# Optimization experiments

Hardware: AMD Instinct MI355X
Metric: run time of the kernel (lower is better)

## Reference

```python
import jax, jax.numpy as jnp
import numpy as np

EPS = 1e-5

def _bn(x, gamma, beta):
    # BatchNorm1d forward (batch statistics, biased variance) over node dim
    mu = x.mean(axis=0)
    var = x.var(axis=0)
    return gamma * (x - mu) * jax.lax.rsqrt(var + EPS) + beta

def _gcn_conv(x, W, b, src, dst, n):
    # PyG GCNConv: h = x @ W; symmetric norm with self-loops; scatter-add to dst
    h = x @ W                                   # [N, out]
    ones = jnp.ones(src.shape, dtype=h.dtype)
    deg = jax.ops.segment_sum(ones, dst, num_segments=n) + 1.0  # +1 self-loop
    dinv = jax.lax.rsqrt(deg)                   # deg >= 1 always
    norm = dinv[src] * dinv[dst]                # [E]
    agg = jax.ops.segment_sum(h[src] * norm[:, None], dst, num_segments=n)
    agg = agg + h * (dinv * dinv)[:, None]      # self-loop contribution
    return agg + b

def setup_inputs() -> dict:
    key = jax.random.key(0)
    ks = jax.random.split(key, 10)
    N, E = 100000, 1600000
    Din, Dh, Dout = 256, 128, 128
    e_prev = jax.random.normal(ks[0], (N, Din), dtype=jnp.float32)
    edge_index = jax.random.randint(ks[1], (2, E), 0, N, dtype=jnp.int64)
    proj_W = jax.random.normal(ks[2], (Din, Din), dtype=jnp.float32) * 0.02
    proj_b = jnp.zeros((Din,), dtype=jnp.float32)
    W1 = jax.random.normal(ks[3], (Din, Dh), dtype=jnp.float32) * 0.05
    b1 = jnp.zeros((Dh,), dtype=jnp.float32)
    gamma1 = jnp.ones((Dh,), dtype=jnp.float32)
    beta1 = jnp.zeros((Dh,), dtype=jnp.float32)
    W2 = jax.random.normal(ks[4], (Dh, Dout), dtype=jnp.float32) * 0.05
    b2 = jnp.zeros((Dout,), dtype=jnp.float32)
    gamma2 = jnp.ones((Dout,), dtype=jnp.float32)
    beta2 = jnp.zeros((Dout,), dtype=jnp.float32)
    return {"e_prev": e_prev, "edge_index": edge_index,
            "proj_W": proj_W, "proj_b": proj_b,
            "W1": W1, "b1": b1, "gamma1": gamma1, "beta1": beta1,
            "W2": W2, "b2": b2, "gamma2": gamma2, "beta2": beta2}

def reference(e_prev, edge_index, proj_W, proj_b, W1, b1, gamma1, beta1, W2, b2, gamma2, beta2):
    n = e_prev.shape[0]
    src, dst = edge_index[0], edge_index[1]
    # input_projection (input_dim != hidden_dim branch)
    x = e_prev @ proj_W + proj_b
    x = _gcn_conv(x, W1, b1, src, dst, n)
    x = _bn(x, gamma1, beta1)
    x = jax.nn.relu(x)
    # dropout(0.2) is identity in eval mode
    x = _gcn_conv(x, W2, b2, src, dst, n)
    x = _bn(x, gamma2, beta2)
    return x
```

## Files before the change

kernel.cpp:

```cpp
#include <hip/hip_runtime.h>
#include <hip/hip_bf16.h>
#include <math.h>

#define BN_EPS 1e-5f
#define CAP 6144
#define MAXB 512

typedef __attribute__((ext_vector_type(8))) short short8;
typedef __attribute__((ext_vector_type(4))) float floatx4;

__device__ inline float4 ntload4(const float* p) {
    floatx4 v = __builtin_nontemporal_load((const floatx4*)p);
    return make_float4(v.x, v.y, v.z, v.w);
}

__global__ __launch_bounds__(128) void prep_kernel(
    const float* __restrict__ PW, const float* __restrict__ W1,
    const float* __restrict__ pb, const float* __restrict__ W2,
    __hip_bfloat16* __restrict__ Wf1, __hip_bfloat16* __restrict__ Wf2,
    float* __restrict__ bc, int* __restrict__ bcursor, int nb)
{
    int bid = blockIdx.x;
    int tid = threadIdx.x;
    if (bid < 256) {
        int k = bid, c = tid;
        float a0 = 0.f, a1 = 0.f, a2 = 0.f, a3 = 0.f;
        for (int kk = 0; kk < 256; kk += 4) {
            a0 = fmaf(PW[k * 256 + kk],     W1[(kk)     * 128 + c], a0);
            a1 = fmaf(PW[k * 256 + kk + 1], W1[(kk + 1) * 128 + c], a1);
            a2 = fmaf(PW[k * 256 + kk + 2], W1[(kk + 2) * 128 + c], a2);
            a3 = fmaf(PW[k * 256 + kk + 3], W1[(kk + 3) * 128 + c], a3);
        }
        float acc = (a0 + a1) + (a2 + a3);
        int kc = k >> 5, r5 = k & 31, qq = r5 >> 3, j = r5 & 7;
        int ct = c >> 4, l16 = c & 15;
        int lane = qq * 16 + l16;
        Wf1[(((kc * 8 + ct) * 64) + lane) * 8 + j] = __float2bfloat16(acc);
    } else if (bid == 256) {
        int c = tid;
        float a0 = 0.f, a1 = 0.f, a2 = 0.f, a3 = 0.f;
        for (int k = 0; k < 256; k += 4) {
            a0 = fmaf(pb[k],     W1[(k)     * 128 + c], a0);
            a1 = fmaf(pb[k + 1], W1[(k + 1) * 128 + c], a1);
            a2 = fmaf(pb[k + 2], W1[(k + 2) * 128 + c], a2);
            a3 = fmaf(pb[k + 3], W1[(k + 3) * 128 + c], a3);
        }
        bc[c] = (a0 + a1) + (a2 + a3);
    } else if (bid < 385) {
        int t = (bid - 257) * 128 + tid;
        int j    = t & 7;
        int lane = (t >> 3) & 63;
        int ct   = (t >> 9) & 7;
        int kc   = t >> 12;
        int k = kc * 32 + ((lane >> 4) & 3) * 8 + j;
        int c = ct * 16 + (lane & 15);
        Wf2[t] = __float2bfloat16(W2[k * 128 + c]);
    } else {
        int i = (bid - 385) * 128 + tid;
        if (i < nb) bcursor[i] = i * CAP;
        if (bid == 385 && tid < 2) bcursor[nb + 8 + tid] = 0;
    }
}

__device__ void bucket_body(
    const int* __restrict__ src, const int* __restrict__ dst,
    int* __restrict__ bcursor, unsigned* __restrict__ buck,
    int E, int nb, int nblocks, int bid)
{
    __shared__ int h[MAXB], resv[MAXB], cur[MAXB];
    for (int t = threadIdx.x; t < nb; t += 256) { h[t] = 0; cur[t] = 0; }
    __syncthreads();
    int per = (E + nblocks - 1) / nblocks;
    int e0 = bid * per;
    int e1 = min(e0 + per, E);
    for (int e = e0 + threadIdx.x; e < e1; e += 256) {
        int d = __builtin_nontemporal_load(&dst[e]);
        atomicAdd(&h[d >> 8], 1);
    }
    __syncthreads();
    for (int t = threadIdx.x; t < nb; t += 256) {
        int c = h[t];
        if (c > 0) resv[t] = atomicAdd(&bcursor[t], c);
    }
    __syncthreads();
    for (int e = e0 + threadIdx.x; e < e1; e += 256) {
        int d = __builtin_nontemporal_load(&dst[e]);
        int s = __builtin_nontemporal_load(&src[e]);
        int b = d >> 8;
        int pos = resv[b] + atomicAdd(&cur[b], 1);
        buck[pos] = ((unsigned)(d & 255) << 17) | (unsigned)s;
    }
}

__global__ __launch_bounds__(256) void csr_kernel(
    const unsigned* __restrict__ buck, const int* __restrict__ bcursor,
    int* __restrict__ cnt, int* __restrict__ rowptr, float* __restrict__ dinv,
    int* __restrict__ ssrc, uint4* __restrict__ Hq, int N)
{
    __shared__ int h[256], sc[256], lcur[256], redu[256];
    __shared__ float sdv[256];
    int b = blockIdx.x;
    int t = threadIdx.x;
    int part = 0;
    for (int i = t; i < b; i += 256) part += bcursor[i] - i * CAP;
    redu[t] = part;
    h[t] = 0;
    __syncthreads();
    for (int off = 128; off > 0; off >>= 1) {
        if (t < off) redu[t] += redu[t + off];
        __syncthreads();
    }
    int cb = redu[0];

    int base = b * CAP;
    int nB = bcursor[b] - base;
    for (int i = t; i < nB; i += 256) {
        unsigned v = buck[base + i];
        atomicAdd(&h[v >> 17], 1);
    }
    __syncthreads();
    int myc = h[t];
    sc[t] = myc;
    __syncthreads();
    for (int off = 1; off < 256; off <<= 1) {
        int x = (t >= off) ? sc[t - off] : 0;
        __syncthreads();
        sc[t] += x;
        __syncthreads();
    }
    int ex = sc[t] - myc;
    lcur[t] = ex;
    int node = b * 256 + t;
    float dv = rsqrtf((float)myc + 1.0f);
    sdv[t] = dv;
    if (node < N) {
        cnt[node]    = myc;
        rowptr[node] = cb + ex;
        dinv[node]   = dv;
    }
    __syncthreads();
    for (int i = t; i < nB; i += 256) {
        unsigned v = buck[base + i];
        int dloc = v >> 17;
        int pos = cb + atomicAdd(&lcur[dloc], 1);
        ssrc[pos] = (int)(v & 0x1FFFFu);
    }
    int rbase = b * 256;
    int nrow  = min(256, N - rbase);
    int l16   = t & 15;
    for (int i = t >> 4; i < nrow; i += 16) {
        float d = sdv[i];
        uint4* rp = &Hq[(size_t)(rbase + i) * 16 + l16];
        uint4 u = *rp;
        uint4 o;
        {
            __hip_bfloat162 p;
            p = __float22bfloat162_rn(make_float2(__uint_as_float(u.x << 16) * d,
                                                  __uint_as_float(u.x & 0xffff0000u) * d));
            o.x = *(unsigned*)&p;
            p = __float22bfloat162_rn(make_float2(__uint_as_float(u.y << 16) * d,
                                                  __uint_as_float(u.y & 0xffff0000u) * d));
            o.y = *(unsigned*)&p;
            p = __float22bfloat162_rn(make_float2(__uint_as_float(u.z << 16) * d,
                                                  __uint_as_float(u.z & 0xffff0000u) * d));
            o.z = *(unsigned*)&p;
            p = __float22bfloat162_rn(make_float2(__uint_as_float(u.w << 16) * d,
                                                  __uint_as_float(u.w & 0xffff0000u) * d));
            o.w = *(unsigned*)&p;
        }
        *rp = o;
    }
}

__device__ inline short8 cvt8(float4 a, float4 b) {
    __hip_bfloat162 p0 = __float22bfloat162_rn(make_float2(a.x, a.y));
    __hip_bfloat162 p1 = __float22bfloat162_rn(make_float2(a.z, a.w));
    __hip_bfloat162 p2 = __float22bfloat162_rn(make_float2(b.x, b.y));
    __hip_bfloat162 p3 = __float22bfloat162_rn(make_float2(b.z, b.w));
    union { short8 s; __hip_bfloat162 h[4]; } u;
    u.h[0] = p0; u.h[1] = p1; u.h[2] = p2; u.h[3] = p3;
    return u.s;
}

template <int K, bool BN, bool DINV>
__device__ void gemm_body(
    int bid,
    const float* __restrict__ X, const short* __restrict__ Wf,
    const float* __restrict__ bias, const float* __restrict__ dinv,
    const float* __restrict__ scale, const float* __restrict__ shift,
    __hip_bfloat16* __restrict__ Hs, int N)
{
    const int wave = threadIdx.x >> 6;
    const int lane = threadIdx.x & 63;
    const int l16  = lane & 15;
    const int q    = lane >> 4;
    const int r0   = bid * 128 + wave * 32;

    const int ra0 = min(r0 + l16, N - 1);
    const int ra1 = min(r0 + 16 + l16, N - 1);
    const float* pA0 = X + (size_t)ra0 * K + q * 8;
    const float* pA1 = X + (size_t)ra1 * K + q * 8;
    const short8* WF = (const short8*)Wf;

    floatx4 acc[2][8];
#pragma unroll
    for (int rt = 0; rt < 2; ++rt)
#pragma unroll
        for (int ct = 0; ct < 8; ++ct) { acc[rt][ct][0] = 0.f; acc[rt][ct][1] = 0.f; acc[rt][ct][2] = 0.f; acc[rt][ct][3] = 0.f; }

#pragma unroll
    for (int kc = 0; kc < K / 32; ++kc) {
        short8 b[8];
#pragma unroll
        for (int ct = 0; ct < 8; ++ct) b[ct] = WF[(kc * 8 + ct) * 64 + lane];

        float4 x00 = ntload4(pA0 + kc * 32);
        float4 x01 = ntload4(pA0 + kc * 32 + 4);
        float4 x10 = ntload4(pA1 + kc * 32);
        float4 x11 = ntload4(pA1 + kc * 32 + 4);
        if (BN) {
            float4 sc0 = *(const float4*)(scale + kc * 32 + q * 8);
            float4 sc1 = *(const float4*)(scale + kc * 32 + q * 8 + 4);
            float4 sh0 = *(const float4*)(shift + kc * 32 + q * 8);
            float4 sh1 = *(const float4*)(shift + kc * 32 + q * 8 + 4);
            x00.x = fmaxf(fmaf(x00.x, sc0.x, sh0.x), 0.f);
            x00.y = fmaxf(fmaf(x00.y, sc0.y, sh0.y), 0.f);
            x00.z = fmaxf(fmaf(x00.z, sc0.z, sh0.z), 0.f);
            x00.w = fmaxf(fmaf(x00.w, sc0.w, sh0.w), 0.f);
            x01.x = fmaxf(fmaf(x01.x, sc1.x, sh1.x), 0.f);
            x01.y = fmaxf(fmaf(x01.y, sc1.y, sh1.y), 0.f);
            x01.z = fmaxf(fmaf(x01.z, sc1.z, sh1.z), 0.f);
            x01.w = fmaxf(fmaf(x01.w, sc1.w, sh1.w), 0.f);
            x10.x = fmaxf(fmaf(x10.x, sc0.x, sh0.x), 0.f);
            x10.y = fmaxf(fmaf(x10.y, sc0.y, sh0.y), 0.f);
            x10.z = fmaxf(fmaf(x10.z, sc0.z, sh0.z), 0.f);
            x10.w = fmaxf(fmaf(x10.w, sc0.w, sh0.w), 0.f);
            x11.x = fmaxf(fmaf(x11.x, sc1.x, sh1.x), 0.f);
            x11.y = fmaxf(fmaf(x11.y, sc1.y, sh1.y), 0.f);
            x11.z = fmaxf(fmaf(x11.z, sc1.z, sh1.z), 0.f);
            x11.w = fmaxf(fmaf(x11.w, sc1.w, sh1.w), 0.f);
        }
        short8 a0 = cvt8(x00, x01);
        short8 a1 = cvt8(x10, x11);
#pragma unroll
        for (int ct = 0; ct < 8; ++ct) {
            acc[0][ct] = __builtin_amdgcn_mfma_f32_16x16x32_bf16(a0, b[ct], acc[0][ct], 0, 0, 0);
            acc[1][ct] = __builtin_amdgcn_mfma_f32_16x16x32_bf16(a1, b[ct], acc[1][ct], 0, 0, 0);
        }
    }

    float bb[8];
#pragma unroll
    for (int ct = 0; ct < 8; ++ct) bb[ct] = bias ? bias[ct * 16 + l16] : 0.f;

#pragma unroll
    for (int rt = 0; rt < 2; ++rt) {
        int rbase = r0 + rt * 16 + q * 4;
        float dv[4];
#pragma unroll
        for (int i = 0; i < 4; ++i) dv[i] = DINV ? dinv[min(rbase + i, N - 1)] : 1.f;
#pragma unroll
        for (int ct = 0; ct < 8; ++ct) {
#pragma unroll
            for (int i = 0; i < 4; ++i) {
                int row = rbase + i;
                if (row < N)
                    Hs[(size_t)row * 128 + ct * 16 + l16] =
                        __float2bfloat16(DINV ? (acc[rt][ct][i] + bb[ct]) * dv[i]
                                              : (acc[rt][ct][i] + bb[ct]));
            }
        }
    }
}

__global__ __launch_bounds__(256) void gemm1_bucket_kernel(
    const float* __restrict__ X, const short* __restrict__ Wf,
    const float* __restrict__ bias,
    __hip_bfloat16* __restrict__ Hs, int N, int gemmGrid,
    const int* __restrict__ src, const int* __restrict__ dst,
    int* __restrict__ bcursor, unsigned* __restrict__ buck, int E, int nb,
    int bucketGrid)
{
    if ((int)blockIdx.x < gemmGrid)
        gemm_body<256, false, false>(blockIdx.x, X, Wf, bias, nullptr, nullptr, nullptr, Hs, N);
    else
        bucket_body(src, dst, bcursor, buck, E, nb, bucketGrid,
                    (int)blockIdx.x - gemmGrid);
}

__global__ __launch_bounds__(256) void mfma_gemm2_kernel(
    const float* __restrict__ X, const short* __restrict__ Wf,
    const float* __restrict__ dinv,
    const float* __restrict__ scale, const float* __restrict__ shift,
    __hip_bfloat16* __restrict__ Hs, int N)
{
    gemm_body<128, true, true>(blockIdx.x, X, Wf, nullptr, dinv, scale, shift, Hs, N);
}

__device__ inline void accrow(uint4 u, float* a) {
    a[0] += __uint_as_float(u.x << 16);
    a[1] += __uint_as_float(u.x & 0xffff0000u);
    a[2] += __uint_as_float(u.y << 16);
    a[3] += __uint_as_float(u.y & 0xffff0000u);
    a[4] += __uint_as_float(u.z << 16);
    a[5] += __uint_as_float(u.z & 0xffff0000u);
    a[6] += __uint_as_float(u.w << 16);
    a[7] += __uint_as_float(u.w & 0xffff0000u);
}

__global__ __launch_bounds__(256) void agg_gather_kernel(
    const uint4* __restrict__ Hq, const int* __restrict__ rowptr,
    const int* __restrict__ cnt, const int* __restrict__ ssrc,
    const float* __restrict__ dinv, const float* __restrict__ bias,
    float* __restrict__ Out, int N)
{
    int node = blockIdx.x * 4 + (threadIdx.x >> 6);
    if (node >= N) return;
    int lane = threadIdx.x & 63;
    int q    = lane >> 4;
    int l16  = lane & 15;

    float a0[8] = {0,0,0,0,0,0,0,0};
    float a1[8] = {0,0,0,0,0,0,0,0};
    float a2[8] = {0,0,0,0,0,0,0,0};
    float a3[8] = {0,0,0,0,0,0,0,0};

    if (q == 0) accrow(Hq[(size_t)node * 16 + l16], a0);

    int start = rowptr[node];
    int num   = cnt[node];
    int j = 0;
    for (; j + 16 <= num; j += 16) {
        int e = start + j + q;
        int s0 = ssrc[e];
        int s1 = ssrc[e + 4];
        int s2 = ssrc[e + 8];
        int s3 = ssrc[e + 12];
        uint4 u0 = Hq[(size_t)s0 * 16 + l16];
        uint4 u1 = Hq[(size_t)s1 * 16 + l16];
        uint4 u2 = Hq[(size_t)s2 * 16 + l16];
        uint4 u3 = Hq[(size_t)s3 * 16 + l16];
        accrow(u0, a0);
        accrow(u1, a1);
        accrow(u2, a2);
        accrow(u3, a3);
    }
    for (; j + 4 <= num; j += 4) {
        int s = ssrc[start + j + q];
        accrow(Hq[(size_t)s * 16 + l16], a0);
    }
    int rem = num - j;
    if (q < rem) {
        int s = ssrc[start + j + q];
        accrow(Hq[(size_t)s * 16 + l16], a1);
    }

#pragma unroll
    for (int i = 0; i < 8; ++i) {
        float v = a0[i] + a1[i] + a2[i] + a3[i];
        v += __shfl_xor(v, 16, 64);
        v += __shfl_xor(v, 32, 64);
        a0[i] = v;
    }

    if (q == 0) {
        float di = dinv[node];
        const float4* B4 = (const float4*)bias;
        float4 bb0 = B4[l16 * 2];
        float4 bb1 = B4[l16 * 2 + 1];
        float4 o0, o1;
        o0.x = fmaf(a0[0], di, bb0.x);
        o0.y = fmaf(a0[1], di, bb0.y);
        o0.z = fmaf(a0[2], di, bb0.z);
        o0.w = fmaf(a0[3], di, bb0.w);
        o1.x = fmaf(a0[4], di, bb1.x);
        o1.y = fmaf(a0[5], di, bb1.y);
        o1.z = fmaf(a0[6], di, bb1.z);
        o1.w = fmaf(a0[7], di, bb1.w);
        float4* O4 = (float4*)(Out + (size_t)node * 128 + l16 * 8);
        O4[0] = o0;
        O4[1] = o1;
    }
}

__global__ __launch_bounds__(256) void bn_stats_kernel(
    const float* __restrict__ A, float* __restrict__ partS, float* __restrict__ partQ,
    int N, int R,
    const float* __restrict__ gamma, const float* __restrict__ beta,
    float* __restrict__ scale, float* __restrict__ shift, int* __restrict__ ctr)
{
    int col4   = threadIdx.x & 31;
    int rowoff = threadIdx.x >> 5;
    int r0 = blockIdx.x * R;
    int r1 = min(r0 + R, N);
    float4 s = make_float4(0.f, 0.f, 0.f, 0.f);
    float4 qq = make_float4(0.f, 0.f, 0.f, 0.f);
#pragma unroll 4
    for (int r = r0 + rowoff; r < r1; r += 8) {
        float4 v = *(const float4*)&A[(size_t)r * 128 + col4 * 4];
        s.x += v.x; s.y += v.y; s.z += v.z; s.w += v.w;
        qq.x = fmaf(v.x, v.x, qq.x);
        qq.y = fmaf(v.y, v.y, qq.y);
        qq.z = fmaf(v.z, v.z, qq.z);
        qq.w = fmaf(v.w, v.w, qq.w);
    }
    __shared__ float4 ls[256], lq[256];
    ls[threadIdx.x] = s;
    lq[threadIdx.x] = qq;
    __syncthreads();
    if (threadIdx.x < 32) {
        float4 ts = ls[threadIdx.x], tq = lq[threadIdx.x];
#pragma unroll
        for (int k = 1; k < 8; ++k) {
            float4 xs = ls[k * 32 + threadIdx.x];
            float4 xq = lq[k * 32 + threadIdx.x];
            ts.x += xs.x; ts.y += xs.y; ts.z += xs.z; ts.w += xs.w;
            tq.x += xq.x; tq.y += xq.y; tq.z += xq.z; tq.w += xq.w;
        }
        *(float4*)&partS[(size_t)blockIdx.x * 128 + threadIdx.x * 4] = ts;
        *(float4*)&partQ[(size_t)blockIdx.x * 128 + threadIdx.x * 4] = tq;
    }
    __syncthreads();
    __shared__ int amLast;
    if (threadIdx.x == 0) {
        __threadfence();
        amLast = (atomicAdd(ctr, 1) == (int)gridDim.x - 1);
    }
    __syncthreads();
    if (!amLast) return;
    __threadfence();
    int c = threadIdx.x & 127;
    int h = threadIdx.x >> 7;
    float fs = 0.f, fq = 0.f;
    for (int b = h * 128; b < h * 128 + 128; ++b) {
        fs += partS[(size_t)b * 128 + c];
        fq += partQ[(size_t)b * 128 + c];
    }
    __shared__ float rs_[256], rq_[256];
    rs_[threadIdx.x] = fs;
    rq_[threadIdx.x] = fq;
    __syncthreads();
    if (threadIdx.x < 128) {
        float S = rs_[threadIdx.x] + rs_[threadIdx.x + 128];
        float Q = rq_[threadIdx.x] + rq_[threadIdx.x + 128];
        float m = S / (float)N;
        float v = Q / (float)N - m * m;
        float rs = rsqrtf(v + BN_EPS);
        float sc = gamma[c] * rs;
        scale[c] = sc;
        shift[c] = fmaf(-m, sc, beta[c]);
    }
}

__global__ void bn_apply_kernel(float* __restrict__ A, const float* __restrict__ scale,
                                const float* __restrict__ shift, int N) {
    int i = blockIdx.x * blockDim.x + threadIdx.x;
    if (i >= N * 32) return;
    int c4 = i & 31;
    float4 v  = ((float4*)A)[i];
    float4 sc = ((const float4*)scale)[c4];
    float4 sh = ((const float4*)shift)[c4];
    v.x = fmaf(v.x, sc.x, sh.x);
    v.y = fmaf(v.y, sc.y, sh.y);
    v.z = fmaf(v.z, sc.z, sh.z);
    v.w = fmaf(v.w, sc.w, sh.w);
    ((float4*)A)[i] = v;
}

extern "C" void kernel_launch(void* const* d_in, const int* in_sizes, int n_in,
                              void* d_out, int out_size, void* d_ws, size_t ws_size,
                              hipStream_t stream) {
    const float* e_prev = (const float*)d_in[0];
    const int*   edges  = (const int*)d_in[1];
    const float* proj_W = (const float*)d_in[2];
    const float* proj_b = (const float*)d_in[3];
    const float* W1     = (const float*)d_in[4];
    const float* b1     = (const float*)d_in[5];
    const float* gamma1 = (const float*)d_in[6];
    const float* beta1  = (const float*)d_in[7];
    const float* W2     = (const float*)d_in[8];
    const float* b2     = (const float*)d_in[9];
    const float* gamma2 = (const float*)d_in[10];
    const float* beta2  = (const float*)d_in[11];
    float* out = (float*)d_out;

    const int N = in_sizes[0] / 256;
    const int E = in_sizes[1] / 2;
    const int* src = edges;
    const int* dst = edges + E;
    const int nb = (N + 255) >> 8;
    const int R = (N + 255) / 256;

    char* p = (char*)d_ws;
    const size_t NH = (size_t)N * 128;
    __hip_bfloat16* Hs = (__hip_bfloat16*)p;  p += NH * 2;
    unsigned* buck  = (unsigned*)p; p += (size_t)nb * CAP * 4;
    int* ssrc   = (int*)p;  p += (size_t)E * 4;
    int* cnt    = (int*)p;  p += (size_t)N * 4;
    int* rowptr = (int*)p;  p += (size_t)N * 4;
    float* dinv = (float*)p; p += (size_t)N * 4;
    int* bcursor = (int*)p; p += (size_t)(nb + 16) * 4;
    float* bc   = (float*)p; p += 128 * 4;
    float* stats = (float*)p; p += 1536 * 4;
    float* partS = (float*)p; p += 256 * 128 * 4;
    float* partQ = (float*)p; p += 256 * 128 * 4;
    __hip_bfloat16* Wf1 = (__hip_bfloat16*)p; p += 256 * 128 * 2;
    __hip_bfloat16* Wf2 = (__hip_bfloat16*)p; p += 128 * 128 * 2;
    float* scale1 = stats, *shift1 = stats + 128;
    float* scale2 = stats + 256, *shift2 = stats + 384;
    int* ctr1 = bcursor + nb + 8;
    int* ctr2 = bcursor + nb + 9;

    const int gemm_grid = (N + 127) / 128;
    const int bucket_grid = 512;

    prep_kernel<<<389, 128, 0, stream>>>(proj_W, W1, proj_b, W2, Wf1, Wf2, bc, bcursor, nb);
    gemm1_bucket_kernel<<<gemm_grid + bucket_grid, 256, 0, stream>>>(
        e_prev, (const short*)Wf1, bc, Hs, N, gemm_grid,
        src, dst, bcursor, buck, E, nb, bucket_grid);
    csr_kernel<<<nb, 256, 0, stream>>>(buck, bcursor, cnt, rowptr, dinv, ssrc,
                                       (uint4*)Hs, N);
    agg_gather_kernel<<<(N + 3) / 4, 256, 0, stream>>>(
        (const uint4*)Hs, rowptr, cnt, ssrc, dinv, b1, out, N);
    bn_stats_kernel<<<256, 256, 0, stream>>>(out, partS, partQ, N, R,
                                             gamma1, beta1, scale1, shift1, ctr1);
    mfma_gemm2_kernel<<<gemm_grid, 256, 0, stream>>>(
        out, (const short*)Wf2, dinv, scale1, shift1, Hs, N);
    agg_gather_kernel<<<(N + 3) / 4, 256, 0, stream>>>(
        (const uint4*)Hs, rowptr, cnt, ssrc, dinv, b2, out, N);
    bn_stats_kernel<<<256, 256, 0, stream>>>(out, partS, partQ, N, R,
                                             gamma2, beta2, scale2, shift2, ctr2);
    bn_apply_kernel<<<(N * 32 + 255) / 256, 256, 0, stream>>>(out, scale2, shift2, N);
}
```

Baseline: 565.4 us.

## Fuse BN statistics into gemm2 and BN2 apply via in-kernel grid barriers

After: 1.059 ms. 1.87x slower.

```diff
diff --git a/kernel.cpp b/kernel.cpp
--- a/kernel.cpp
+++ b/kernel.cpp
@@ -5,6 +5,7 @@
 #define BN_EPS 1e-5f
 #define CAP 6144
 #define MAXB 512
+#define PSTRIDE 1024
 
 typedef __attribute__((ext_vector_type(8))) short short8;
 typedef __attribute__((ext_vector_type(4))) float floatx4;
@@ -58,7 +59,7 @@
     } else {
         int i = (bid - 385) * 128 + tid;
         if (i < nb) bcursor[i] = i * CAP;
-        if (bid == 385 && tid < 2) bcursor[nb + 8 + tid] = 0;
+        if (bid == 385 && tid < 4) bcursor[nb + 8 + tid] = 0;
     }
 }
 
@@ -74,7 +75,7 @@
     int e0 = bid * per;
     int e1 = min(e0 + per, E);
     for (int e = e0 + threadIdx.x; e < e1; e += 256) {
-        int d = __builtin_nontemporal_load(&dst[e]);
+        int d = dst[e];
         atomicAdd(&h[d >> 8], 1);
     }
     __syncthreads();
@@ -84,8 +85,8 @@
     }
     __syncthreads();
     for (int e = e0 + threadIdx.x; e < e1; e += 256) {
-        int d = __builtin_nontemporal_load(&dst[e]);
-        int s = __builtin_nontemporal_load(&src[e]);
+        int d = dst[e];
+        int s = src[e];
         int b = d >> 8;
         int pos = resv[b] + atomicAdd(&cur[b], 1);
         buck[pos] = ((unsigned)(d & 255) << 17) | (unsigned)s;
@@ -273,6 +274,70 @@
     }
 }
 
+__device__ void bn_partials_body(
+    const float* __restrict__ A, float* __restrict__ pS, float* __restrict__ pQ,
+    int r0, int r1, int bid)
+{
+    int col4   = threadIdx.x & 31;
+    int rowoff = threadIdx.x >> 5;
+    float4 s = make_float4(0.f, 0.f, 0.f, 0.f);
+    float4 qq = make_float4(0.f, 0.f, 0.f, 0.f);
+#pragma unroll 4
+    for (int r = r0 + rowoff; r < r1; r += 8) {
+        float4 v = *(const float4*)&A[(size_t)r * 128 + col4 * 4];
+        s.x += v.x; s.y += v.y; s.z += v.z; s.w += v.w;
+        qq.x = fmaf(v.x, v.x, qq.x);
+        qq.y = fmaf(v.y, v.y, qq.y);
+        qq.z = fmaf(v.z, v.z, qq.z);
+        qq.w = fmaf(v.w, v.w, qq.w);
+    }
+    __shared__ float4 ls[256], lq[256];
+    ls[threadIdx.x] = s;
+    lq[threadIdx.x] = qq;
+    __syncthreads();
+    if (threadIdx.x < 32) {
+        float4 ts = ls[threadIdx.x], tq = lq[threadIdx.x];
+#pragma unroll
+        for (int k = 1; k < 8; ++k) {
+            float4 xs = ls[k * 32 + threadIdx.x];
+            float4 xq = lq[k * 32 + threadIdx.x];
+            ts.x += xs.x; ts.y += xs.y; ts.z += xs.z; ts.w += xs.w;
+            tq.x += xq.x; tq.y += xq.y; tq.z += xq.z; tq.w += xq.w;
+        }
+        int c = threadIdx.x * 4;
+        pS[(size_t)(c + 0) * PSTRIDE + bid] = ts.x;
+        pS[(size_t)(c + 1) * PSTRIDE + bid] = ts.y;
+        pS[(size_t)(c + 2) * PSTRIDE + bid] = ts.z;
+        pS[(size_t)(c + 3) * PSTRIDE + bid] = ts.w;
+        pQ[(size_t)(c + 0) * PSTRIDE + bid] = tq.x;
+        pQ[(size_t)(c + 1) * PSTRIDE + bid] = tq.y;
+        pQ[(size_t)(c + 2) * PSTRIDE + bid] = tq.z;
+        pQ[(size_t)(c + 3) * PSTRIDE + bid] = tq.w;
+    }
+    __syncthreads();
+}
+
+__device__ void bn_finalize_body(
+    const float* __restrict__ pS, const float* __restrict__ pQ, int nbk,
+    const float* __restrict__ gamma, const float* __restrict__ beta,
+    float* __restrict__ scale, float* __restrict__ shift, int N)
+{
+    int t = threadIdx.x;
+    if (t < 128) {
+        float fs = 0.f, fq = 0.f;
+        const float* ps = pS + (size_t)t * PSTRIDE;
+        const float* pq = pQ + (size_t)t * PSTRIDE;
+        for (int b = 0; b < nbk; ++b) { fs += ps[b]; fq += pq[b]; }
+        float m = fs / (float)N;
+        float v = fq / (float)N - m * m;
+        float rs = rsqrtf(v + BN_EPS);
+        float sc = gamma[t] * rs;
+        scale[t] = sc;
+        shift[t] = fmaf(-m, sc, beta[t]);
+    }
+    __syncthreads();
+}
+
 __global__ __launch_bounds__(256) void gemm1_bucket_kernel(
     const float* __restrict__ X, const short* __restrict__ Wf,
     const float* __restrict__ bias,
@@ -288,13 +353,77 @@
                     (int)blockIdx.x - gemmGrid);
 }
 
-__global__ __launch_bounds__(256) void mfma_gemm2_kernel(
+__global__ __launch_bounds__(256, 4) void gemm2_bn1_kernel(
     const float* __restrict__ X, const short* __restrict__ Wf,
     const float* __restrict__ dinv,
-    const float* __restrict__ scale, const float* __restrict__ shift,
+    const float* __restrict__ gamma, const float* __restrict__ beta,
+    float* __restrict__ pS, float* __restrict__ pQ,
+    float* __restrict__ scale, float* __restrict__ shift,
+    int* __restrict__ ctr, int* __restrict__ flag,
     __hip_bfloat16* __restrict__ Hs, int N)
 {
-    gemm_body<128, true, true>(blockIdx.x, X, Wf, nullptr, dinv, scale, shift, Hs, N);
+    const int nbk = (int)gridDim.x;
+    const int bid = blockIdx.x;
+    {
+        int RR = (N + nbk - 1) / nbk;
+        int r0 = bid * RR;
+        int r1 = min(r0 + RR, N);
+        bn_partials_body(X, pS, pQ, r0, r1, bid);
+        if (threadIdx.x == 0) { __threadfence(); atomicAdd(ctr, 1); }
+    }
+    if (bid == 0) {
+        if (threadIdx.x == 0)
+            while (atomicAdd(ctr, 0) < nbk) __builtin_amdgcn_s_sleep(8);
+        __syncthreads();
+        __threadfence();
+        bn_finalize_body(pS, pQ, nbk, gamma, beta, scale, shift, N);
+        if (threadIdx.x == 0) { __threadfence(); atomicAdd(flag, 1); }
+    }
+    if (threadIdx.x == 0)
+        while (atomicAdd(flag, 0) < 1) __builtin_amdgcn_s_sleep(8);
+    __syncthreads();
+    __threadfence();
+    gemm_body<128, true, true>(bid, X, Wf, nullptr, dinv, scale, shift, Hs, N);
+}
+
+__global__ __launch_bounds__(256, 8) void bn2_tail_kernel(
+    float* __restrict__ A, float* __restrict__ pS, float* __restrict__ pQ,
+    const float* __restrict__ gamma, const float* __restrict__ beta,
+    float* __restrict__ scale, float* __restrict__ shift,
+    int* __restrict__ ctr, int* __restrict__ flag, int N)
+{
+    const int nbk = (int)gridDim.x;
+    const int bid = blockIdx.x;
+    const int RR = (N + nbk - 1) / nbk;
+    const int r0 = bid * RR;
+    const int r1 = min(r0 + RR, N);
+    bn_partials_body(A, pS, pQ, r0, r1, bid);
+    if (threadIdx.x == 0) { __threadfence(); atomicAdd(ctr, 1); }
+    if (bid == 0) {
+        if (threadIdx.x == 0)
+            while (atomicAdd(ctr, 0) < nbk) __builtin_amdgcn_s_sleep(8);
+        __syncthreads();
+        __threadfence();
+        bn_finalize_body(pS, pQ, nbk, gamma, beta, scale, shift, N);
+        if (threadIdx.x == 0) { __threadfence(); atomicAdd(flag, 1); }
+    }
+    if (threadIdx.x == 0)
+        while (atomicAdd(flag, 0) < 1) __builtin_amdgcn_s_sleep(8);
+    __syncthreads();
+    __threadfence();
+    int col4   = threadIdx.x & 31;
+    int rowoff = threadIdx.x >> 5;
+    float4 sc = ((const float4*)scale)[col4];
+    float4 sh = ((const float4*)shift)[col4];
+    for (int r = r0 + rowoff; r < r1; r += 8) {
+        float4* pv = (float4*)&A[(size_t)r * 128 + col4 * 4];
+        float4 v = *pv;
+        v.x = fmaf(v.x, sc.x, sh.x);
+        v.y = fmaf(v.y, sc.y, sh.y);
+        v.z = fmaf(v.z, sc.z, sh.z);
+        v.w = fmaf(v.w, sc.w, sh.w);
+        *pv = v;
+    }
 }
 
 __device__ inline void accrow(uint4 u, float* a) {
@@ -383,90 +512,6 @@
     }
 }
 
-__global__ __launch_bounds__(256) void bn_stats_kernel(
-    const float* __restrict__ A, float* __restrict__ partS, float* __restrict__ partQ,
-    int N, int R,
-    const float* __restrict__ gamma, const float* __restrict__ beta,
-    float* __restrict__ scale, float* __restrict__ shift, int* __restrict__ ctr)
-{
-    int col4   = threadIdx.x & 31;
-    int rowoff = threadIdx.x >> 5;
-    int r0 = blockIdx.x * R;
-    int r1 = min(r0 + R, N);
-    float4 s = make_float4(0.f, 0.f, 0.f, 0.f);
-    float4 qq = make_float4(0.f, 0.f, 0.f, 0.f);
-#pragma unroll 4
-    for (int r = r0 + rowoff; r < r1; r += 8) {
-        float4 v = *(const float4*)&A[(size_t)r * 128 + col4 * 4];
-        s.x += v.x; s.y += v.y; s.z += v.z; s.w += v.w;
-        qq.x = fmaf(v.x, v.x, qq.x);
-        qq.y = fmaf(v.y, v.y, qq.y);
-        qq.z = fmaf(v.z, v.z, qq.z);
-        qq.w = fmaf(v.w, v.w, qq.w);
-    }
-    __shared__ float4 ls[256], lq[256];
-    ls[threadIdx.x] = s;
-    lq[threadIdx.x] = qq;
-    __syncthreads();
-    if (threadIdx.x < 32) {
-        float4 ts = ls[threadIdx.x], tq = lq[threadIdx.x];
-#pragma unroll
-        for (int k = 1; k < 8; ++k) {
-            float4 xs = ls[k * 32 + threadIdx.x];
-            float4 xq = lq[k * 32 + threadIdx.x];
-            ts.x += xs.x; ts.y += xs.y; ts.z += xs.z; ts.w += xs.w;
-            tq.x += xq.x; tq.y += xq.y; tq.z += xq.z; tq.w += xq.w;
-        }
-        *(float4*)&partS[(size_t)blockIdx.x * 128 + threadIdx.x * 4] = ts;
-        *(float4*)&partQ[(size_t)blockIdx.x * 128 + threadIdx.x * 4] = tq;
-    }
-    __syncthreads();
-    __shared__ int amLast;
-    if (threadIdx.x == 0) {
-        __threadfence();
-        amLast = (atomicAdd(ctr, 1) == (int)gridDim.x - 1);
-    }
-    __syncthreads();
-    if (!amLast) return;
-    __threadfence();
-    int c = threadIdx.x & 127;
-    int h = threadIdx.x >> 7;
-    float fs = 0.f, fq = 0.f;
-    for (int b = h * 128; b < h * 128 + 128; ++b) {
-        fs += partS[(size_t)b * 128 + c];
-        fq += partQ[(size_t)b * 128 + c];
-    }
-    __shared__ float rs_[256], rq_[256];
-    rs_[threadIdx.x] = fs;
-    rq_[threadIdx.x] = fq;
-    __syncthreads();
-    if (threadIdx.x < 128) {
-        float S = rs_[threadIdx.x] + rs_[threadIdx.x + 128];
-        float Q = rq_[threadIdx.x] + rq_[threadIdx.x + 128];
-        float m = S / (float)N;
-        float v = Q / (float)N - m * m;
-        float rs = rsqrtf(v + BN_EPS);
-        float sc = gamma[c] * rs;
-        scale[c] = sc;
-        shift[c] = fmaf(-m, sc, beta[c]);
-    }
-}
-
-__global__ void bn_apply_kernel(float* __restrict__ A, const float* __restrict__ scale,
-                                const float* __restrict__ shift, int N) {
-    int i = blockIdx.x * blockDim.x + threadIdx.x;
-    if (i >= N * 32) return;
-    int c4 = i & 31;
-    float4 v  = ((float4*)A)[i];
-    float4 sc = ((const float4*)scale)[c4];
-    float4 sh = ((const float4*)shift)[c4];
-    v.x = fmaf(v.x, sc.x, sh.x);
-    v.y = fmaf(v.y, sc.y, sh.y);
-    v.z = fmaf(v.z, sc.z, sh.z);
-    v.w = fmaf(v.w, sc.w, sh.w);
-    ((float4*)A)[i] = v;
-}
-
 extern "C" void kernel_launch(void* const* d_in, const int* in_sizes, int n_in,
                               void* d_out, int out_size, void* d_ws, size_t ws_size,
                               hipStream_t stream) {
@@ -489,7 +534,6 @@
     const int* src = edges;
     const int* dst = edges + E;
     const int nb = (N + 255) >> 8;
-    const int R = (N + 255) / 256;
 
     char* p = (char*)d_ws;
     const size_t NH = (size_t)N * 128;
@@ -502,14 +546,16 @@
     int* bcursor = (int*)p; p += (size_t)(nb + 16) * 4;
     float* bc   = (float*)p; p += 128 * 4;
     float* stats = (float*)p; p += 1536 * 4;
-    float* partS = (float*)p; p += 256 * 128 * 4;
-    float* partQ = (float*)p; p += 256 * 128 * 4;
+    float* partS = (float*)p; p += (size_t)128 * PSTRIDE * 4;
+    float* partQ = (float*)p; p += (size_t)128 * PSTRIDE * 4;
     __hip_bfloat16* Wf1 = (__hip_bfloat16*)p; p += 256 * 128 * 2;
     __hip_bfloat16* Wf2 = (__hip_bfloat16*)p; p += 128 * 128 * 2;
     float* scale1 = stats, *shift1 = stats + 128;
     float* scale2 = stats + 256, *shift2 = stats + 384;
-    int* ctr1 = bcursor + nb + 8;
-    int* ctr2 = bcursor + nb + 9;
+    int* ctrA  = bcursor + nb + 8;
+    int* flagA = bcursor + nb + 9;
+    int* ctrB  = bcursor + nb + 10;
+    int* flagB = bcursor + nb + 11;
 
     const int gemm_grid = (N + 127) / 128;
     const int bucket_grid = 512;
@@ -522,13 +568,11 @@
                                        (uint4*)Hs, N);
     agg_gather_kernel<<<(N + 3) / 4, 256, 0, stream>>>(
         (const uint4*)Hs, rowptr, cnt, ssrc, dinv, b1, out, N);
-    bn_stats_kernel<<<256, 256, 0, stream>>>(out, partS, partQ, N, R,
-                                             gamma1, beta1, scale1, shift1, ctr1);
-    mfma_gemm2_kernel<<<gemm_grid, 256, 0, stream>>>(
-        out, (const short*)Wf2, dinv, scale1, shift1, Hs, N);
+    gemm2_bn1_kernel<<<gemm_grid, 256, 0, stream>>>(
+        out, (const short*)Wf2, dinv, gamma1, beta1,
+        partS, partQ, scale1, shift1, ctrA, flagA, Hs, N);
     agg_gather_kernel<<<(N + 3) / 4, 256, 0, stream>>>(
         (const uint4*)Hs, rowptr, cnt, ssrc, dinv, b2, out, N);
-    bn_stats_kernel<<<256, 256, 0, stream>>>(out, partS, partQ, N, R,
-                                             gamma2, beta2, scale2, shift2, ctr2);
-    bn_apply_kernel<<<(N * 32 + 255) / 256, 256, 0, stream>>>(out, scale2, shift2, N);
-}
+    bn2_tail_kernel<<<1024, 256, 0, stream>>>(
+        out, partS, partQ, gamma2, beta2, scale2, shift2, ctrB, flagB, N);
+}
```

## Slice bf16 feature matrix into column blocks for cache-resident gather aggregation

Applied to the files above, without the earlier changes.

After: 866.7 us. 1.53x slower.

```diff
diff --git a/kernel.cpp b/kernel.cpp
--- a/kernel.cpp
+++ b/kernel.cpp
@@ -74,7 +74,7 @@
     int e0 = bid * per;
     int e1 = min(e0 + per, E);
     for (int e = e0 + threadIdx.x; e < e1; e += 256) {
-        int d = __builtin_nontemporal_load(&dst[e]);
+        int d = dst[e];
         atomicAdd(&h[d >> 8], 1);
     }
     __syncthreads();
@@ -84,18 +84,31 @@
     }
     __syncthreads();
     for (int e = e0 + threadIdx.x; e < e1; e += 256) {
-        int d = __builtin_nontemporal_load(&dst[e]);
-        int s = __builtin_nontemporal_load(&src[e]);
+        int d = dst[e];
+        int s = src[e];
         int b = d >> 8;
         int pos = resv[b] + atomicAdd(&cur[b], 1);
         buck[pos] = ((unsigned)(d & 255) << 17) | (unsigned)s;
     }
 }
 
+__device__ inline uint2 scale_u2(uint2 v, float d) {
+    float f0 = __uint_as_float(v.x << 16) * d;
+    float f1 = __uint_as_float(v.x & 0xffff0000u) * d;
+    float f2 = __uint_as_float(v.y << 16) * d;
+    float f3 = __uint_as_float(v.y & 0xffff0000u) * d;
+    __hip_bfloat162 p0 = __float22bfloat162_rn(make_float2(f0, f1));
+    __hip_bfloat162 p1 = __float22bfloat162_rn(make_float2(f2, f3));
+    uint2 o;
+    o.x = *(unsigned*)&p0;
+    o.y = *(unsigned*)&p1;
+    return o;
+}
+
 __global__ __launch_bounds__(256) void csr_kernel(
     const unsigned* __restrict__ buck, const int* __restrict__ bcursor,
     int* __restrict__ cnt, int* __restrict__ rowptr, float* __restrict__ dinv,
-    int* __restrict__ ssrc, uint4* __restrict__ Hq, int N)
+    int* __restrict__ ssrc, uint2* __restrict__ HU, int N)
 {
     __shared__ int h[256], sc[256], lcur[256], redu[256];
     __shared__ float sdv[256];
@@ -147,28 +160,13 @@
     }
     int rbase = b * 256;
     int nrow  = min(256, N - rbase);
-    int l16   = t & 15;
-    for (int i = t >> 4; i < nrow; i += 16) {
-        float d = sdv[i];
-        uint4* rp = &Hq[(size_t)(rbase + i) * 16 + l16];
-        uint4 u = *rp;
-        uint4 o;
-        {
-            __hip_bfloat162 p;
-            p = __float22bfloat162_rn(make_float2(__uint_as_float(u.x << 16) * d,
-                                                  __uint_as_float(u.x & 0xffff0000u) * d));
-            o.x = *(unsigned*)&p;
-            p = __float22bfloat162_rn(make_float2(__uint_as_float(u.y << 16) * d,
-                                                  __uint_as_float(u.y & 0xffff0000u) * d));
-            o.y = *(unsigned*)&p;
-            p = __float22bfloat162_rn(make_float2(__uint_as_float(u.z << 16) * d,
-                                                  __uint_as_float(u.z & 0xffff0000u) * d));
-            o.z = *(unsigned*)&p;
-            p = __float22bfloat162_rn(make_float2(__uint_as_float(u.w << 16) * d,
-                                                  __uint_as_float(u.w & 0xffff0000u) * d));
-            o.w = *(unsigned*)&p;
-        }
-        *rp = o;
+    for (int s2 = 0; s2 < 8; ++s2) {
+        for (int i = t; i < nrow * 4; i += 256) {
+            int row = i >> 2;
+            int uu  = i & 3;
+            size_t a = ((size_t)s2 * N + rbase + row) * 4 + uu;
+            HU[a] = scale_u2(HU[a], sdv[row]);
+        }
     }
 }
 
@@ -265,7 +263,7 @@
             for (int i = 0; i < 4; ++i) {
                 int row = rbase + i;
                 if (row < N)
-                    Hs[(size_t)row * 128 + ct * 16 + l16] =
+                    Hs[((size_t)ct * N + row) * 16 + l16] =
                         __float2bfloat16(DINV ? (acc[rt][ct][i] + bb[ct]) * dv[i]
                                               : (acc[rt][ct][i] + bb[ct]));
             }
@@ -297,89 +295,60 @@
     gemm_body<128, true, true>(blockIdx.x, X, Wf, nullptr, dinv, scale, shift, Hs, N);
 }
 
-__device__ inline void accrow(uint4 u, float* a) {
-    a[0] += __uint_as_float(u.x << 16);
-    a[1] += __uint_as_float(u.x & 0xffff0000u);
-    a[2] += __uint_as_float(u.y << 16);
-    a[3] += __uint_as_float(u.y & 0xffff0000u);
-    a[4] += __uint_as_float(u.z << 16);
-    a[5] += __uint_as_float(u.z & 0xffff0000u);
-    a[6] += __uint_as_float(u.w << 16);
-    a[7] += __uint_as_float(u.w & 0xffff0000u);
-}
-
 __global__ __launch_bounds__(256) void agg_gather_kernel(
-    const uint4* __restrict__ Hq, const int* __restrict__ rowptr,
+    const uint2* __restrict__ HU, const int* __restrict__ rowptr,
     const int* __restrict__ cnt, const int* __restrict__ ssrc,
     const float* __restrict__ dinv, const float* __restrict__ bias,
     float* __restrict__ Out, int N)
 {
-    int node = blockIdx.x * 4 + (threadIdx.x >> 6);
-    if (node >= N) return;
-    int lane = threadIdx.x & 63;
-    int q    = lane >> 4;
-    int l16  = lane & 15;
-
-    float a0[8] = {0,0,0,0,0,0,0,0};
-    float a1[8] = {0,0,0,0,0,0,0,0};
-    float a2[8] = {0,0,0,0,0,0,0,0};
-    float a3[8] = {0,0,0,0,0,0,0,0};
-
-    if (q == 0) accrow(Hq[(size_t)node * 16 + l16], a0);
-
-    int start = rowptr[node];
-    int num   = cnt[node];
-    int j = 0;
-    for (; j + 16 <= num; j += 16) {
-        int e = start + j + q;
-        int s0 = ssrc[e];
-        int s1 = ssrc[e + 4];
-        int s2 = ssrc[e + 8];
-        int s3 = ssrc[e + 12];
-        uint4 u0 = Hq[(size_t)s0 * 16 + l16];
-        uint4 u1 = Hq[(size_t)s1 * 16 + l16];
-        uint4 u2 = Hq[(size_t)s2 * 16 + l16];
-        uint4 u3 = Hq[(size_t)s3 * 16 + l16];
-        accrow(u0, a0);
-        accrow(u1, a1);
-        accrow(u2, a2);
-        accrow(u3, a3);
-    }
-    for (; j + 4 <= num; j += 4) {
-        int s = ssrc[start + j + q];
-        accrow(Hq[(size_t)s * 16 + l16], a0);
-    }
-    int rem = num - j;
-    if (q < rem) {
-        int s = ssrc[start + j + q];
-        accrow(Hq[(size_t)s * 16 + l16], a1);
-    }
-
-#pragma unroll
-    for (int i = 0; i < 8; ++i) {
-        float v = a0[i] + a1[i] + a2[i] + a3[i];
-        v += __shfl_xor(v, 16, 64);
-        v += __shfl_xor(v, 32, 64);
-        a0[i] = v;
-    }
-
-    if (q == 0) {
-        float di = dinv[node];
-        const float4* B4 = (const float4*)bias;
-        float4 bb0 = B4[l16 * 2];
-        float4 bb1 = B4[l16 * 2 + 1];
-        float4 o0, o1;
-        o0.x = fmaf(a0[0], di, bb0.x);
-        o0.y = fmaf(a0[1], di, bb0.y);
-        o0.z = fmaf(a0[2], di, bb0.z);
-        o0.w = fmaf(a0[3], di, bb0.w);
-        o1.x = fmaf(a0[4], di, bb1.x);
-        o1.y = fmaf(a0[5], di, bb1.y);
-        o1.z = fmaf(a0[6], di, bb1.z);
-        o1.w = fmaf(a0[7], di, bb1.w);
-        float4* O4 = (float4*)(Out + (size_t)node * 128 + l16 * 8);
-        O4[0] = o0;
-        O4[1] = o1;
+    const int s        = blockIdx.x & 7;
+    const int nodeBase = (blockIdx.x >> 3) * 16;
+    const int w        = threadIdx.x >> 6;
+    const int lane     = threadIdx.x & 63;
+    const int g        = lane >> 2;
+    const int u        = lane & 3;
+    const size_t sliceOff = (size_t)s * N;
+
+    const float4 bb = *(const float4*)(bias + s * 16 + u * 4);
+
+#pragma unroll
+    for (int nn = 0; nn < 4; ++nn) {
+        int n = nodeBase + w * 4 + nn;
+        if (n < N) {
+            float a0 = 0.f, a1 = 0.f, a2 = 0.f, a3 = 0.f;
+            if (g == 0) {
+                uint2 v = HU[(sliceOff + n) * 4 + u];
+                a0 += __uint_as_float(v.x << 16);
+                a1 += __uint_as_float(v.x & 0xffff0000u);
+                a2 += __uint_as_float(v.y << 16);
+                a3 += __uint_as_float(v.y & 0xffff0000u);
+            }
+            int start = rowptr[n];
+            int num   = cnt[n];
+            for (int j = g; j < num; j += 16) {
+                int sidx = ssrc[start + j];
+                uint2 v = HU[(sliceOff + sidx) * 4 + u];
+                a0 += __uint_as_float(v.x << 16);
+                a1 += __uint_as_float(v.x & 0xffff0000u);
+                a2 += __uint_as_float(v.y << 16);
+                a3 += __uint_as_float(v.y & 0xffff0000u);
+            }
+            for (int off = 4; off < 64; off <<= 1) {
+                a0 += __shfl_xor(a0, off, 64);
+                a1 += __shfl_xor(a1, off, 64);
+                a2 += __shfl_xor(a2, off, 64);
+                a3 += __shfl_xor(a3, off, 64);
+            }
+            if (g == 0) {
+                float di = dinv[n];
+                float4 o;
+                o.x = fmaf(a0, di, bb.x);
+                o.y = fmaf(a1, di, bb.y);
+                o.z = fmaf(a2, di, bb.z);
+                o.w = fmaf(a3, di, bb.w);
+                *(float4*)(Out + (size_t)n * 128 + s * 16 + u * 4) = o;
+            }
+        }
     }
 }
 
@@ -513,21 +482,22 @@
 
     const int gemm_grid = (N + 127) / 128;
     const int bucket_grid = 512;
+    const int agg_grid = ((N + 15) / 16) * 8;
 
     prep_kernel<<<389, 128, 0, stream>>>(proj_W, W1, proj_b, W2, Wf1, Wf2, bc, bcursor, nb);
     gemm1_bucket_kernel<<<gemm_grid + bucket_grid, 256, 0, stream>>>(
         e_prev, (const short*)Wf1, bc, Hs, N, gemm_grid,
         src, dst, bcursor, buck, E, nb, bucket_grid);
     csr_kernel<<<nb, 256, 0, stream>>>(buck, bcursor, cnt, rowptr, dinv, ssrc,
-                                       (uint4*)Hs, N);
-    agg_gather_kernel<<<(N + 3) / 4, 256, 0, stream>>>(
-        (const uint4*)Hs, rowptr, cnt, ssrc, dinv, b1, out, N);
+                                       (uint2*)Hs, N);
+    agg_gather_kernel<<<agg_grid, 256, 0, stream>>>(
+        (const uint2*)Hs, rowptr, cnt, ssrc, dinv, b1, out, N);
     bn_stats_kernel<<<256, 256, 0, stream>>>(out, partS, partQ, N, R,
                                              gamma1, beta1, scale1, shift1, ctr1);
     mfma_gemm2_kernel<<<gemm_grid, 256, 0, stream>>>(
         out, (const short*)Wf2, dinv, scale1, shift1, Hs, N);
-    agg_gather_kernel<<<(N + 3) / 4, 256, 0, stream>>>(
-        (const uint4*)Hs, rowptr, cnt, ssrc, dinv, b2, out, N);
+    agg_gather_kernel<<<agg_grid, 256, 0, stream>>>(
+        (const uint2*)Hs, rowptr, cnt, ssrc, dinv, b2, out, N);
     bn_stats_kernel<<<256, 256, 0, stream>>>(out, partS, partQ, N, R,
                                              gamma2, beta2, scale2, shift2, ctr2);
     bn_apply_kernel<<<(N * 32 + 255) / 256, 256, 0, stream>>>(out, scale2, shift2, N);
```
